# Kernel optimization log

Hardware: AMD Instinct MI355X
Metric: run time of the kernel (lower is better)

Reference implementation:

```python
import jax, jax.numpy as jnp
import numpy as np

NUM_CLASSES = 10
HIDDEN = 64
_LABEL2MASK_THRESHOL = 500


def setup_inputs() -> dict:
    key = jax.random.key(0)
    ks = jax.random.split(key, 5)
    B, h, w = 4, 60, 80
    feature1 = jax.random.normal(ks[0], (B, 512, h, w), jnp.float32)
    feature2 = jax.random.normal(ks[1], (B, 512, h // 2, w // 2), jnp.float32)
    # kaiming_normal (fan_in, relu): std = sqrt(2 / fan_in)
    w1 = jax.random.normal(ks[2], (HIDDEN, 512), jnp.float32) * np.sqrt(2.0 / 512)
    w2 = jax.random.normal(ks[3], (HIDDEN, 512), jnp.float32) * np.sqrt(2.0 / 512)
    wc = jax.random.normal(ks[4], (NUM_CLASSES + 1, HIDDEN), jnp.float32) * np.sqrt(2.0 / HIDDEN)
    b1 = jnp.zeros((HIDDEN,), jnp.float32)
    b2 = jnp.zeros((HIDDEN,), jnp.float32)
    bc = jnp.zeros((NUM_CLASSES + 1,), jnp.float32)
    return {"feature1": feature1, "feature2": feature2, "w1": w1, "b1": b1,
            "w2": w2, "b2": b2, "wc": wc, "bc": bc}


def _conv1x1(x, w, b):
    # x: (B,C,H,W), w: (O,C), b: (O,)
    return jnp.einsum('bchw,oc->bohw', x, w) + b[None, :, None, None]


def _resize2x(x, s):
    B, C, H, W = x.shape
    # torch nn.Upsample(mode='bilinear', align_corners=False) == half-pixel bilinear
    return jax.image.resize(x, (B, C, H * s, W * s), method='bilinear')


def _label2bbx(seg, num_classes, thresh):
    # seg: (B,H,W) int. Fixed-shape, fully vectorized version of the nested
    # python-loop bbox extraction. Rows with pixel count < thresh are -1.
    B, H, W = seg.shape
    cls = jnp.arange(1, num_classes, dtype=seg.dtype)        # skip background cls 0
    mask = seg[:, None, :, :] == cls[None, :, None, None]    # (B,K,H,W)
    cnt = mask.sum(axis=(2, 3))
    xs = jnp.arange(W, dtype=jnp.int32)[None, None, None, :]
    ys = jnp.arange(H, dtype=jnp.int32)[None, None, :, None]
    x1 = jnp.min(jnp.where(mask, xs, W), axis=(2, 3))
    x2 = jnp.max(jnp.where(mask, xs, -1), axis=(2, 3))
    y1 = jnp.min(jnp.where(mask, ys, H), axis=(2, 3))
    y2 = jnp.max(jnp.where(mask, ys, -1), axis=(2, 3))
    K = num_classes - 1
    bid = jnp.broadcast_to(jnp.arange(B, dtype=jnp.int32)[:, None], (B, K))
    cid = jnp.broadcast_to(cls.astype(jnp.int32)[None, :], (B, K))
    rows = jnp.stack([bid, x1.astype(jnp.int32), y1.astype(jnp.int32),
                      x2.astype(jnp.int32), y2.astype(jnp.int32), cid], axis=-1)  # (B,K,6)
    valid = (cnt >= thresh)[..., None]
    rows = jnp.where(valid, rows, -1)
    return rows.reshape(B * K, 6)


def reference(feature1, feature2, w1, b1, w2, b2, wc, bc):
    f1 = jax.nn.relu(_conv1x1(feature1, w1, b1))
    f2 = jax.nn.relu(_conv1x1(feature2, w2, b2))
    f2 = _resize2x(f2, 2)
    feat = _resize2x(f1 + f2, 8)              # (B,64,480,640)
    logits = _conv1x1(feat, wc, bc)           # (B,11,480,640)
    probability = jax.nn.softmax(logits, axis=1)
    segmentation = jnp.argmax(probability, axis=1)
    bbx = _label2bbx(segmentation, NUM_CLASSES, _LABEL2MASK_THRESHOL)
    return probability, segmentation, bbx
```

## Files before the change

kernel.cpp:

```cpp
#include <hip/hip_runtime.h>

#define BN 4
#define CIN 512
#define H1 60
#define W1 80
#define P1 4800
#define H2 30
#define W2 40
#define P2 1200
#define HID 64
#define NCLS 11
#define HF 480
#define WF 640
#define PF 307200
#define THRESH 500

#define WT1_OFF 0
#define WT2_OFF 32768
#define F2_OFF  65536
#define PART_OFF F2_OFF
#define L_OFF   (65536 + 307200)

__device__ __forceinline__ void dma16(const float* g, float* l) {
    __builtin_amdgcn_global_load_lds(
        (const __attribute__((address_space(1))) void*)g,
        (__attribute__((address_space(3))) void*)l, 16, 0, 0);
}

__global__ void k0_init(const float* __restrict__ w1, const float* __restrict__ w2,
                        float* __restrict__ ws) {
    int idx = blockIdx.x * 256 + threadIdx.x;
    if (idx < 32768) {
        int c = idx >> 6, o = idx & 63;
        ws[WT1_OFF + idx] = w1[o * CIN + c];
    } else {
        int j = idx - 32768;
        int c = j >> 6, o = j & 63;
        ws[WT2_OFF + j] = w2[o * CIN + c];
    }
}

__global__ __launch_bounds__(256, 4) void k1_conv2(const float* __restrict__ x,
                                                   const float* __restrict__ b2,
                                                   float* __restrict__ ws) {
    __shared__ float lds[8320];
    const float* wt = ws + WT2_OFF;
    float* f2o = ws + F2_OFF;
    int blk = blockIdx.x;
    int b = blk / 150, tile = blk % 150;
    int t = threadIdx.x;
    int l = t & 63, w = t >> 6;
    int q = t & 1, og = (t >> 1) & 7, ch = t >> 4;
    int o0 = og * 8;
    int p0 = tile * 8;
    const float* xb = x + (size_t)b * CIN * P2 + p0;

    auto stage = [&](int s) {
        int buf = s & 1;
#pragma unroll
        for (int j = 0; j < 2; ++j) {
            int r0 = j * 128 + w * 32;
            int r  = r0 + (l >> 1);
            int cg = (r >> 4) * 32 + s * 16 + (r & 15);
            dma16(xb + (size_t)cg * P2 + (l & 1) * 4,
                  lds + buf * 2048 + r0 * 8);
        }
    };

    float acc[4][8];
#pragma unroll
    for (int j = 0; j < 4; ++j)
#pragma unroll
        for (int i = 0; i < 8; ++i) acc[j][i] = 0.f;

    stage(0);
    __syncthreads();
    const float* wp = wt + (ch * 32) * HID + o0;
    for (int s = 0; s < 2; ++s) {
        if (s < 1) stage(s + 1);
        const float* xs = lds + (s & 1) * 2048 + ch * 128 + q * 4;
#pragma unroll 4
        for (int cc = 0; cc < 16; ++cc) {
            float4 xv = *(const float4*)(xs + cc * 8);
            const float* wr = wp + (s * 16 + cc) * HID;
            float4 wa = *(const float4*)(wr);
            float4 wb = *(const float4*)(wr + 4);
            float w8[8] = {wa.x, wa.y, wa.z, wa.w, wb.x, wb.y, wb.z, wb.w};
            float x4[4] = {xv.x, xv.y, xv.z, xv.w};
#pragma unroll
            for (int j = 0; j < 4; ++j)
#pragma unroll
                for (int i = 0; i < 8; ++i) acc[j][i] = fmaf(w8[i], x4[j], acc[j][i]);
        }
        __syncthreads();
    }
#pragma unroll
    for (int j = 0; j < 4; ++j)
#pragma unroll
        for (int i = 0; i < 8; ++i)
            lds[ch * 520 + (q * 4 + j) * 65 + o0 + i] = acc[j][i];
    __syncthreads();

    if (t < 64) {
        int px = t >> 3, oo = (t & 7) * 8;
        float v[8];
#pragma unroll
        for (int i = 0; i < 8; ++i) {
            float s = 0.f;
#pragma unroll
            for (int c = 0; c < 16; ++c) s += lds[c * 520 + px * 65 + oo + i];
            v[i] = fmaxf(s + b2[oo + i], 0.f);
        }
        float* outp = f2o + ((size_t)b * P2 + p0 + px) * HID + oo;
        *(float4*)outp = make_float4(v[0], v[1], v[2], v[3]);
        *(float4*)(outp + 4) = make_float4(v[4], v[5], v[6], v[7]);
    }
}

__global__ __launch_bounds__(256, 4) void k2_conv1(const float* __restrict__ x,
                                                   const float* __restrict__ b1,
                                                   const float* __restrict__ wc,
                                                   const float* __restrict__ bc,
                                                   float* __restrict__ ws) {
    __shared__ float lds[8320];
    const float* wt = ws + WT1_OFF;
    const float* f2 = ws + F2_OFF;
    float* lout = ws + L_OFF;
    int blk = blockIdx.x;
    int b = blk / 300, tile = blk % 300;
    int t = threadIdx.x;
    int l = t & 63, w = t >> 6;
    int q = t & 3, og = (t >> 2) & 7, ch = t >> 5;
    int o0 = og * 8;
    int p0 = tile * 16;
    const float* xb = x + (size_t)b * CIN * P1 + p0;

    auto stage = [&](int s) {
        int buf = s & 1;
#pragma unroll
        for (int j = 0; j < 4; ++j) {
            int r0 = j * 64 + w * 16;
            int r  = r0 + (l >> 2);
            int cg = (r >> 5) * 64 + s * 32 + (r & 31);
            dma16(xb + (size_t)cg * P1 + (l & 3) * 4,
                  lds + buf * 4096 + r0 * 16);
        }
    };

    float acc[4][8];
#pragma unroll
    for (int j = 0; j < 4; ++j)
#pragma unroll
        for (int i = 0; i < 8; ++i) acc[j][i] = 0.f;

    stage(0);
    __syncthreads();
    const float* wp = wt + (ch * 64) * HID + o0;
    for (int s = 0; s < 2; ++s) {
        if (s < 1) stage(s + 1);
        const float* xs = lds + (s & 1) * 4096 + ch * 512 + q * 4;
#pragma unroll 4
        for (int cc = 0; cc < 32; ++cc) {
            float4 xv = *(const float4*)(xs + cc * 16);
            const float* wr = wp + (s * 32 + cc) * HID;
            float4 wa = *(const float4*)(wr);
            float4 wb = *(const float4*)(wr + 4);
            float w8[8] = {wa.x, wa.y, wa.z, wa.w, wb.x, wb.y, wb.z, wb.w};
            float x4[4] = {xv.x, xv.y, xv.z, xv.w};
#pragma unroll
            for (int j = 0; j < 4; ++j)
#pragma unroll
                for (int i = 0; i < 8; ++i) acc[j][i] = fmaf(w8[i], x4[j], acc[j][i]);
        }
        __syncthreads();
    }
#pragma unroll
    for (int j = 0; j < 4; ++j)
#pragma unroll
        for (int i = 0; i < 8; ++i)
            lds[ch * 1040 + (q * 4 + j) * 65 + o0 + i] = acc[j][i];
    __syncthreads();

    if (t < 128) {
        int px = t >> 3;
        int oo = (t & 7) * 8;
        int p = p0 + px;
        int y = p / W1, xq = p - y * W1;
        float sy = fmaf((float)y, 0.5f, -0.25f);
        float fy = floorf(sy);
        float ty = sy - fy;
        int y0 = max(0, min(H2 - 1, (int)fy));
        int y1 = max(0, min(H2 - 1, (int)fy + 1));
        float sx = fmaf((float)xq, 0.5f, -0.25f);
        float fx = floorf(sx);
        float tx = sx - fx;
        int x0 = max(0, min(W2 - 1, (int)fx));
        int x1 = max(0, min(W2 - 1, (int)fx + 1));
        float wy0 = 1.f - ty, wx0 = 1.f - tx;
        const float* f2b = f2 + (size_t)b * P2 * HID;
        const float* r00 = f2b + (y0 * W2 + x0) * HID + oo;
        const float* r01 = f2b + (y0 * W2 + x1) * HID + oo;
        const float* r10 = f2b + (y1 * W2 + x0) * HID + oo;
        const float* r11 = f2b + (y1 * W2 + x1) * HID + oo;
#pragma unroll
        for (int i = 0; i < 8; ++i) {
            int a = px * 65 + oo + i;
            float s = lds[a] + lds[1040 + a] + lds[2 * 1040 + a] + lds[3 * 1040 + a]
                    + lds[4 * 1040 + a] + lds[5 * 1040 + a] + lds[6 * 1040 + a] + lds[7 * 1040 + a];
            float f1v = fmaxf(s + b1[oo + i], 0.f);
            float v0 = r00[i] * wx0 + r01[i] * tx;
            float v1 = r10[i] * wx0 + r11[i] * tx;
            lds[a] = f1v + (v0 * wy0 + v1 * ty);
        }
    }
    __syncthreads();

    {
        int px2 = t & 15;
        int kg = t >> 4;
        if (kg < 11) {
            float l1 = bc[kg];
#pragma unroll 8
            for (int o = 0; o < HID; ++o) {
                float gv = lds[px2 * 65 + o];
                l1 = fmaf(wc[kg * HID + o], gv, l1);
            }
            lout[((size_t)b * P1 + p0 + px2) * 12 + kg] = l1;
        } else if (kg == 11) {
            lout[((size_t)b * P1 + p0 + px2) * 12 + 11] = 0.f;
        }
    }
}

__global__ __launch_bounds__(256) void k4_main(float* __restrict__ out,
                                               float* __restrict__ ws) {
    __shared__ int s_cnt[9], s_x0[9], s_y0[9], s_x1[9], s_y1[9];
    const float* l = ws + L_OFF;
    int* partb = (int*)(ws + PART_OFF);
    int t = threadIdx.x;
    if (t < 9) { s_cnt[t] = 0; s_x0[t] = WF; s_y0[t] = HF; s_x1[t] = -1; s_y1[t] = -1; }
    __syncthreads();

    int fl = blockIdx.x * 256 + t;
    int b = fl / PF;
    int r = fl - b * PF;
    int Y = r / WF;
    int X = r - Y * WF;

    float sy = fmaf((float)Y, 0.125f, -0.4375f);
    float fy = floorf(sy);
    float ty = sy - fy;
    int y0 = max(0, min(H1 - 1, (int)fy));
    int y1 = max(0, min(H1 - 1, (int)fy + 1));
    float sx = fmaf((float)X, 0.125f, -0.4375f);
    float fx = floorf(sx);
    float tx = sx - fx;
    int x0 = max(0, min(W1 - 1, (int)fx));
    int x1 = max(0, min(W1 - 1, (int)fx + 1));
    float wy0 = 1.f - ty, wx0 = 1.f - tx;

    const float* lb = l + (size_t)b * P1 * 12;
    const float4* q00 = (const float4*)(lb + (y0 * W1 + x0) * 12);
    const float4* q01 = (const float4*)(lb + (y0 * W1 + x1) * 12);
    const float4* q10 = (const float4*)(lb + (y1 * W1 + x0) * 12);
    const float4* q11 = (const float4*)(lb + (y1 * W1 + x1) * 12);
    float l00[12], l01[12], l10[12], l11[12];
#pragma unroll
    for (int j = 0; j < 3; ++j) {
        ((float4*)l00)[j] = q00[j];
        ((float4*)l01)[j] = q01[j];
        ((float4*)l10)[j] = q10[j];
        ((float4*)l11)[j] = q11[j];
    }
    float li[11];
#pragma unroll
    for (int k = 0; k < 11; ++k) {
        float v0 = l00[k] * wx0 + l01[k] * tx;
        float v1 = l10[k] * wx0 + l11[k] * tx;
        li[k] = v0 * wy0 + v1 * ty;
    }
    int am = 0;
    float bm = li[0];
#pragma unroll
    for (int k = 1; k < 11; ++k) {
        if (li[k] > bm) { bm = li[k]; am = k; }
    }
    float e[11];
    float s = 0.f;
#pragma unroll
    for (int k = 0; k < 11; ++k) { e[k] = __expf(li[k] - bm); s += e[k]; }
    float rs = 1.f / s;
    size_t ob = (size_t)b * NCLS * PF + r;
#pragma unroll
    for (int k = 0; k < 11; ++k) out[ob + (size_t)k * PF] = e[k] * rs;
    out[(size_t)BN * NCLS * PF + fl] = (float)am;

    int lane = t & 63;
    int X0 = X & ~63;
    for (int c = 1; c <= 9; ++c) {
        unsigned long long m = __ballot(am == c);
        if (m != 0ULL && lane == 0) {
            int ci = c - 1;
            atomicAdd(&s_cnt[ci], (int)__popcll(m));
            atomicMin(&s_x0[ci], X0 + __builtin_ctzll(m));
            atomicMax(&s_x1[ci], X0 + 63 - __builtin_clzll(m));
            atomicMin(&s_y0[ci], Y);
            atomicMax(&s_y1[ci], Y);
        }
    }
    __syncthreads();
    if (t < 9) {
        int* pr = partb + blockIdx.x * 45 + t * 5;
        pr[0] = s_cnt[t];
        pr[1] = s_x0[t];
        pr[2] = s_y0[t];
        pr[3] = s_x1[t];
        pr[4] = s_y1[t];
    }
}

__global__ void k5_bbx(float* __restrict__ out, const float* __restrict__ ws) {
    const int* partb = (const int*)(ws + PART_OFF);
    int b = blockIdx.x / 9, c = blockIdx.x % 9;
    int t = threadIdx.x;
    int cnt = 0, mnx = WF, mny = HF, mxx = -1, mxy = -1;
    for (int i = t; i < 1200; i += 64) {
        const int* pr = partb + (size_t)(b * 1200 + i) * 45 + c * 5;
        cnt += pr[0];
        mnx = min(mnx, pr[1]);
        mny = min(mny, pr[2]);
        mxx = max(mxx, pr[3]);
        mxy = max(mxy, pr[4]);
    }
    for (int sft = 32; sft; sft >>= 1) {
        cnt += __shfl_xor(cnt, sft);
        mnx = min(mnx, __shfl_xor(mnx, sft));
        mny = min(mny, __shfl_xor(mny, sft));
        mxx = max(mxx, __shfl_xor(mxx, sft));
        mxy = max(mxy, __shfl_xor(mxy, sft));
    }
    if (t == 0) {
        float* row = out + (size_t)BN * NCLS * PF + (size_t)BN * PF + (size_t)(b * 9 + c) * 6;
        bool ok = cnt >= THRESH;
        row[0] = ok ? (float)b : -1.f;
        row[1] = ok ? (float)mnx : -1.f;
        row[2] = ok ? (float)mny : -1.f;
        row[3] = ok ? (float)mxx : -1.f;
        row[4] = ok ? (float)mxy : -1.f;
        row[5] = ok ? (float)(c + 1) : -1.f;
    }
}

extern "C" void kernel_launch(void* const* d_in, const int* in_sizes, int n_in,
                              void* d_out, int out_size, void* d_ws, size_t ws_size,
                              hipStream_t stream) {
    const float* f1 = (const float*)d_in[0];
    const float* f2 = (const float*)d_in[1];
    const float* w1 = (const float*)d_in[2];
    const float* b1 = (const float*)d_in[3];
    const float* w2 = (const float*)d_in[4];
    const float* b2 = (const float*)d_in[5];
    const float* wc = (const float*)d_in[6];
    const float* bc = (const float*)d_in[7];
    float* out = (float*)d_out;
    float* ws = (float*)d_ws;

    k0_init<<<dim3(256), dim3(256), 0, stream>>>(w1, w2, ws);
    k1_conv2<<<dim3(600), dim3(256), 0, stream>>>(f2, b2, ws);
    k2_conv1<<<dim3(1200), dim3(256), 0, stream>>>(f1, b1, wc, bc, ws);
    k4_main<<<dim3(4800), dim3(256), 0, stream>>>(out, ws);
    k5_bbx<<<dim3(36), dim3(64), 0, stream>>>(out, ws);
}
```

Before: 171.5 us.

## Split conv1 into channel-half partial-sum kernel and separate reduce/classifier kernel

The fused conv1 kernel becomes two kernels. The first computes 32-pixel tiles over half of the 512 input channels and writes partial sums to a new workspace region. The second adds the two halves, applies bias and ReLU, adds the bilinear-upsampled f2, and runs the 11-class classifier, with each thread now handling two classes. The aim is wider pixel tiles for better reuse of weight loads and a classifier stage without a mostly idle tail, at the cost of an extra launch and a global round-trip for the partial sums.

```diff
diff --git a/kernel.cpp b/kernel.cpp
--- a/kernel.cpp
+++ b/kernel.cpp
@@ -20,6 +20,7 @@
 #define F2_OFF  65536
 #define PART_OFF F2_OFF
 #define L_OFF   (65536 + 307200)
+#define PP_OFF  603136
 
 __device__ __forceinline__ void dma16(const float* g, float* l) {
     __builtin_amdgcn_global_load_lds(
@@ -117,33 +118,32 @@
     }
 }
 
-__global__ __launch_bounds__(256, 4) void k2_conv1(const float* __restrict__ x,
-                                                   const float* __restrict__ b1,
-                                                   const float* __restrict__ wc,
-                                                   const float* __restrict__ bc,
-                                                   float* __restrict__ ws) {
+__global__ __launch_bounds__(256, 4) void k2a_conv1(const float* __restrict__ x,
+                                                    float* __restrict__ ws) {
     __shared__ float lds[8320];
     const float* wt = ws + WT1_OFF;
-    const float* f2 = ws + F2_OFF;
-    float* lout = ws + L_OFF;
+    float* pp = ws + PP_OFF;
     int blk = blockIdx.x;
-    int b = blk / 300, tile = blk % 300;
+    int b = blk / 300;
+    int rem = blk - b * 300;
+    int hb = rem / 150;
+    int tile = rem - hb * 150;
     int t = threadIdx.x;
     int l = t & 63, w = t >> 6;
-    int q = t & 3, og = (t >> 2) & 7, ch = t >> 5;
+    int q = t & 7, og = (t >> 3) & 7, ch = t >> 6;
     int o0 = og * 8;
-    int p0 = tile * 16;
-    const float* xb = x + (size_t)b * CIN * P1 + p0;
+    int p0 = tile * 32;
+    const float* xb = x + (size_t)b * CIN * P1 + (size_t)hb * 256 * P1 + p0;
 
     auto stage = [&](int s) {
         int buf = s & 1;
 #pragma unroll
         for (int j = 0; j < 4; ++j) {
-            int r0 = j * 64 + w * 16;
-            int r  = r0 + (l >> 2);
+            int r0 = j * 32 + w * 8;
+            int r  = r0 + (l >> 3);
             int cg = (r >> 5) * 64 + s * 32 + (r & 31);
-            dma16(xb + (size_t)cg * P1 + (l & 3) * 4,
-                  lds + buf * 4096 + r0 * 16);
+            dma16(xb + (size_t)cg * P1 + (l & 7) * 4,
+                  lds + buf * 4096 + r0 * 32);
         }
     };
 
@@ -155,13 +155,13 @@
 
     stage(0);
     __syncthreads();
-    const float* wp = wt + (ch * 64) * HID + o0;
+    const float* wp = wt + (size_t)(hb * 256 + ch * 64) * HID + o0;
     for (int s = 0; s < 2; ++s) {
         if (s < 1) stage(s + 1);
-        const float* xs = lds + (s & 1) * 4096 + ch * 512 + q * 4;
+        const float* xs = lds + (s & 1) * 4096 + ch * 1024 + q * 4;
 #pragma unroll 4
         for (int cc = 0; cc < 32; ++cc) {
-            float4 xv = *(const float4*)(xs + cc * 16);
+            float4 xv = *(const float4*)(xs + cc * 32);
             const float* wr = wp + (s * 32 + cc) * HID;
             float4 wa = *(const float4*)(wr);
             float4 wb = *(const float4*)(wr + 4);
@@ -178,13 +178,50 @@
     for (int j = 0; j < 4; ++j)
 #pragma unroll
         for (int i = 0; i < 8; ++i)
-            lds[ch * 1040 + (q * 4 + j) * 65 + o0 + i] = acc[j][i];
-    __syncthreads();
-
-    if (t < 128) {
+            lds[ch * 2080 + (q * 4 + j) * 65 + o0 + i] = acc[j][i];
+    __syncthreads();
+
+    {
+        int px = t >> 3;
+        int oo = (t & 7) * 8;
+        float v[8];
+#pragma unroll
+        for (int i = 0; i < 8; ++i) {
+            int a = px * 65 + oo + i;
+            v[i] = lds[a] + lds[2080 + a] + lds[2 * 2080 + a] + lds[3 * 2080 + a];
+        }
+        float* outp = pp + ((size_t)(b * 2 + hb) * P1 + p0 + px) * HID + oo;
+        *(float4*)outp = make_float4(v[0], v[1], v[2], v[3]);
+        *(float4*)(outp + 4) = make_float4(v[4], v[5], v[6], v[7]);
+    }
+}
+
+__global__ __launch_bounds__(256) void k2b_reduce(const float* __restrict__ b1,
+                                                  const float* __restrict__ wc,
+                                                  const float* __restrict__ bc,
+                                                  float* __restrict__ ws) {
+    __shared__ float g[2080];
+    const float* pp = ws + PP_OFF;
+    const float* f2 = ws + F2_OFF;
+    float* lout = ws + L_OFF;
+    int blk = blockIdx.x;
+    int b = blk / 150, tile = blk % 150;
+    int t = threadIdx.x;
+    int p0 = tile * 32;
+
+    {
         int px = t >> 3;
         int oo = (t & 7) * 8;
         int p = p0 + px;
+        const float* h0 = pp + ((size_t)(b * 2 + 0) * P1 + p) * HID + oo;
+        const float* h1 = pp + ((size_t)(b * 2 + 1) * P1 + p) * HID + oo;
+        float4 a0 = *(const float4*)h0;
+        float4 a1 = *(const float4*)(h0 + 4);
+        float4 c0 = *(const float4*)h1;
+        float4 c1 = *(const float4*)(h1 + 4);
+        float hs[8] = {a0.x + c0.x, a0.y + c0.y, a0.z + c0.z, a0.w + c0.w,
+                       a1.x + c1.x, a1.y + c1.y, a1.z + c1.z, a1.w + c1.w};
+
         int y = p / W1, xq = p - y * W1;
         float sy = fmaf((float)y, 0.5f, -0.25f);
         float fy = floorf(sy);
@@ -204,31 +241,30 @@
         const float* r11 = f2b + (y1 * W2 + x1) * HID + oo;
 #pragma unroll
         for (int i = 0; i < 8; ++i) {
-            int a = px * 65 + oo + i;
-            float s = lds[a] + lds[1040 + a] + lds[2 * 1040 + a] + lds[3 * 1040 + a]
-                    + lds[4 * 1040 + a] + lds[5 * 1040 + a] + lds[6 * 1040 + a] + lds[7 * 1040 + a];
-            float f1v = fmaxf(s + b1[oo + i], 0.f);
+            float f1v = fmaxf(hs[i] + b1[oo + i], 0.f);
             float v0 = r00[i] * wx0 + r01[i] * tx;
             float v1 = r10[i] * wx0 + r11[i] * tx;
-            lds[a] = f1v + (v0 * wy0 + v1 * ty);
+            g[px * 65 + oo + i] = f1v + (v0 * wy0 + v1 * ty);
         }
     }
     __syncthreads();
 
     {
-        int px2 = t & 15;
-        int kg = t >> 4;
-        if (kg < 11) {
-            float l1 = bc[kg];
+        int px2 = t & 31;
+        int kg = t >> 5;
+        int k2i = (kg < 3) ? kg + 8 : 8;
+        float l1 = bc[kg];
+        float l2 = bc[k2i];
 #pragma unroll 8
-            for (int o = 0; o < HID; ++o) {
-                float gv = lds[px2 * 65 + o];
-                l1 = fmaf(wc[kg * HID + o], gv, l1);
-            }
-            lout[((size_t)b * P1 + p0 + px2) * 12 + kg] = l1;
-        } else if (kg == 11) {
-            lout[((size_t)b * P1 + p0 + px2) * 12 + 11] = 0.f;
-        }
+        for (int o = 0; o < HID; ++o) {
+            float gv = g[px2 * 65 + o];
+            l1 = fmaf(wc[kg * HID + o], gv, l1);
+            l2 = fmaf(wc[k2i * HID + o], gv, l2);
+        }
+        float* lrow = lout + ((size_t)b * P1 + p0 + px2) * 12;
+        lrow[kg] = l1;
+        if (kg < 3) lrow[kg + 8] = l2;
+        else if (kg == 3) lrow[11] = 0.f;
     }
 }
 
@@ -367,7 +403,8 @@
 
     k0_init<<<dim3(256), dim3(256), 0, stream>>>(w1, w2, ws);
     k1_conv2<<<dim3(600), dim3(256), 0, stream>>>(f2, b2, ws);
-    k2_conv1<<<dim3(1200), dim3(256), 0, stream>>>(f1, b1, wc, bc, ws);
+    k2a_conv1<<<dim3(1200), dim3(256), 0, stream>>>(f1, ws);
+    k2b_reduce<<<dim3(600), dim3(256), 0, stream>>>(b1, wc, bc, ws);
     k4_main<<<dim3(4800), dim3(256), 0, stream>>>(out, ws);
     k5_bbx<<<dim3(36), dim3(64), 0, stream>>>(out, ws);
 }
```

Result: no change. 173.4 us (+1.1%).
